# Performance work log

Hardware: AMD Instinct MI355X
Metric: run time of the kernel (lower is better)

The kernel has to match this reference:

```python
import jax, jax.numpy as jnp
import numpy as np

WS = 7        # window_size
SHIFT = 3     # shift_size
HEADS = 6
DIM = 192
HIDDEN = DIM * 6  # mlp_ratio=6
EPS = 1e-5


def _rel_pos_index(ws):
    # static relative-position index, (ws*ws, ws*ws) int
    coords = np.stack(np.meshgrid(np.arange(ws), np.arange(ws), indexing='ij')).reshape(2, -1)
    rel = coords[:, :, None] - coords[:, None, :]            # (2, N, N)
    rel = rel.transpose(1, 2, 0)                             # (N, N, 2)
    rel[:, :, 0] += ws - 1
    rel[:, :, 1] += ws - 1
    rel[:, :, 0] *= 2 * ws - 1
    return rel.sum(-1)


def _layernorm(t, g, b):
    m = t.mean(-1, keepdims=True)
    v = jnp.mean((t - m) ** 2, axis=-1, keepdims=True)
    return (t - m) * jax.lax.rsqrt(v + EPS) * g + b


def setup_inputs() -> dict:
    key = jax.random.key(0)
    ks = jax.random.split(key, 8)
    B, H, W = 16, 56, 56
    x = jax.random.normal(ks[0], (B, H * W, DIM), dtype=jnp.float32)
    p = lambda k, s: (jax.random.normal(k, s, dtype=jnp.float32) * 0.02)
    return {
        'x': x, 'H': H, 'W': W,
        'ln1_g': jnp.ones((DIM,), jnp.float32), 'ln1_b': jnp.zeros((DIM,), jnp.float32),
        'qkv_w': p(ks[1], (3 * DIM, DIM)), 'qkv_b': jnp.zeros((3 * DIM,), jnp.float32),
        'rpb': p(ks[2], ((2 * WS - 1) ** 2, HEADS)),
        'proj_w': p(ks[3], (DIM, DIM)), 'proj_b': jnp.zeros((DIM,), jnp.float32),
        'ln2_g': jnp.ones((DIM,), jnp.float32), 'ln2_b': jnp.zeros((DIM,), jnp.float32),
        'fc1_w': p(ks[4], (HIDDEN, DIM)), 'fc1_b': jnp.zeros((HIDDEN,), jnp.float32),
        'fc2_w': p(ks[5], (DIM, HIDDEN)), 'fc2_b': jnp.zeros((DIM,), jnp.float32),
    }


def reference(x, H, W, ln1_g, ln1_b, qkv_w, qkv_b, rpb, proj_w, proj_b,
              ln2_g, ln2_b, fc1_w, fc1_b, fc2_w, fc2_b):
    B, L, C = x.shape
    hd = C // HEADS
    shortcut = x
    h = _layernorm(x, ln1_g, ln1_b).reshape(B, H, W, C)
    pad_r = (WS - W % WS) % WS
    pad_b = (WS - H % WS) % WS
    h = jnp.pad(h, ((0, 0), (0, pad_b), (0, pad_r), (0, 0)))
    Hp, Wp = H + pad_b, W + pad_r
    if SHIFT > 0:
        h = jnp.roll(h, (-SHIFT, -SHIFT), axis=(1, 2))
    # window partition -> (nW*B, WS*WS, C)
    h = h.reshape(B, Hp // WS, WS, Wp // WS, WS, C).transpose(0, 1, 3, 2, 4, 5)
    h = h.reshape(-1, WS * WS, C)
    nB, N, _ = h.shape
    qkv = (h @ qkv_w.T + qkv_b).reshape(nB, N, 3, HEADS, hd).transpose(2, 0, 3, 1, 4)
    q, k, v = qkv[0], qkv[1], qkv[2]       # (nB, heads, N, hd)
    scale = hd ** -0.5
    attn = jnp.einsum('bhnd,bhmd->bhnm', q * scale, k)
    idx = _rel_pos_index(WS)
    bias = rpb[idx.reshape(-1)].reshape(N, N, HEADS).transpose(2, 0, 1)  # (heads, N, N)
    attn = jax.nn.softmax(attn + bias[None], axis=-1)
    out = jnp.einsum('bhnm,bhmd->bhnd', attn, v).transpose(0, 2, 1, 3).reshape(nB, N, C)
    out = out @ proj_w.T + proj_b
    # window reverse -> (B, Hp, Wp, C)
    out = out.reshape(B, Hp // WS, Wp // WS, WS, WS, C).transpose(0, 1, 3, 2, 4, 5)
    out = out.reshape(B, Hp, Wp, C)
    if SHIFT > 0:
        out = jnp.roll(out, (SHIFT, SHIFT), axis=(1, 2))
    out = out[:, :H, :W, :].reshape(B, H * W, C)
    x = shortcut + out
    h2 = _layernorm(x, ln2_g, ln2_b)
    h2 = jax.nn.gelu(h2 @ fc1_w.T + fc1_b, approximate=False)
    return x + (h2 @ fc2_w.T + fc2_b)
```

## Files before the change

### kernel.cpp

```cpp
#include <hip/hip_runtime.h>

typedef unsigned short u16;
typedef __bf16 bf16x8 __attribute__((ext_vector_type(8)));
typedef __bf16 bf16x2_t __attribute__((ext_vector_type(2)));
typedef float f32x4 __attribute__((ext_vector_type(4)));

#define AS1 __attribute__((address_space(1)))
#define AS3 __attribute__((address_space(3)))

__device__ __forceinline__ void gld16(const void* g, void* l) {
  __builtin_amdgcn_global_load_lds((const AS1 void*)g, (AS3 void*)l, 16, 0, 0);
}

__device__ __forceinline__ u16 f2bf(float f) {
  union { float f; unsigned int u; } v; v.f = f;
  unsigned int u = v.u;
  u += 0x7fffu + ((u >> 16) & 1u);
  return (u16)(u >> 16);
}
__device__ __forceinline__ float bf2f(u16 h) {
  union { unsigned int u; float f; } v; v.u = ((unsigned int)h) << 16; return v.f;
}
__device__ __forceinline__ unsigned int pk2(float a, float b) {
#if __has_builtin(__builtin_amdgcn_cvt_pk_bf16_f32)
  union { bf16x2_t v; unsigned int u; } c;
  c.v = __builtin_amdgcn_cvt_pk_bf16_f32(a, b);
  return c.u;
#else
  return (unsigned int)f2bf(a) | ((unsigned int)f2bf(b) << 16);
#endif
}
__device__ __forceinline__ float gelu_f(float v) {
  float u = v * (1.5957691216f + 0.0713548163f * v * v);
  return v * __builtin_amdgcn_rcpf(1.0f + __expf(-u));
}

__global__ __launch_bounds__(256) void cast_weights(
    const float* __restrict__ w0, const float* __restrict__ w1,
    const float* __restrict__ w2, const float* __restrict__ w3,
    u16* __restrict__ o0, u16* __restrict__ o1,
    u16* __restrict__ o2, u16* __restrict__ o3) {
  int i = blockIdx.x * 256 + threadIdx.x;
  if (i < 110592) o0[i] = f2bf(w0[i]);
  if (i < 36864) {
    int n = i / 192, kp = i - n * 192;
    int h = kp >> 5, dp = kp & 31;
    int d = (dp & 1) ? ((dp >> 1) + 16) : (dp >> 1);
    o1[i] = f2bf(w1[n * 192 + h * 32 + d]);
  }
  if (i < 221184) o2[i] = f2bf(w2[i]);
  if (i < 221184) o3[i] = f2bf(w3[i]);
}

__global__ __launch_bounds__(256) void build_btab(
    const float* __restrict__ rpb, float* __restrict__ btab) {
  int id = blockIdx.x * 256 + threadIdx.x;
  int head = id >> 12;
  int m = (id >> 6) & 63;
  int r = id & 63;
  float v;
  if (m >= 49) v = -1e30f;
  else if (r >= 49) v = 0.0f;
  else {
    int mi = m / 7, mj = m - mi * 7;
    int ri = r / 7, rj = r - ri * 7;
    v = rpb[((ri - mi + 6) * 13 + (rj - mj + 6)) * 6 + head];
  }
  btab[id] = v;
}

__global__ __launch_bounds__(256) void ln_kernel(
    const float* __restrict__ x, const float* __restrict__ g,
    const float* __restrict__ b, u16* __restrict__ out) {
  int row = blockIdx.x * 4 + (threadIdx.x >> 6);
  int lane = threadIdx.x & 63;
  const float* xr = x + (long)row * 192;
  float e0 = xr[lane], e1 = xr[lane + 64], e2 = xr[lane + 128];
  float s = e0 + e1 + e2;
  #pragma unroll
  for (int o = 1; o < 64; o <<= 1) s += __shfl_xor(s, o);
  float mean = s * (1.0f / 192.0f);
  float d0 = e0 - mean, d1 = e1 - mean, d2 = e2 - mean;
  float q = d0 * d0 + d1 * d1 + d2 * d2;
  #pragma unroll
  for (int o = 1; o < 64; o <<= 1) q += __shfl_xor(q, o);
  float rstd = rsqrtf(q * (1.0f / 192.0f) + 1e-5f);
  u16* orow = out + (long)row * 192;
  orow[lane]       = f2bf(d0 * rstd * g[lane]       + b[lane]);
  orow[lane + 64]  = f2bf(d1 * rstd * g[lane + 64]  + b[lane + 64]);
  orow[lane + 128] = f2bf(d2 * rstd * g[lane + 128] + b[lane + 128]);
}

template<int MODE>
__global__ __launch_bounds__(256, 4) void gemm_kernel(
    const u16* __restrict__ A, const u16* __restrict__ W,
    const float* __restrict__ bias, const float* __restrict__ resid,
    void* __restrict__ out, int N, int K) {
  __shared__ u16 lds[2 * 7168];
  float* ct = (float*)lds;
  const int tid = threadIdx.x;
  const int wave = tid >> 6, lane = tid & 63;
  const int wm = wave >> 1, wn = wave & 1;
  const int quad = lane >> 4, l15 = lane & 15;
  const long bm = (long)blockIdx.x * 128;
  const int bn = blockIdx.y * 96;
  const int NC = K >> 5;

  for (int t = wave; t < 14; t += 4) {
    const u16* g = (t < 8)
        ? (A + (bm + t * 16 + l15) * K + quad * 8)
        : (W + (long)(bn + (t - 8) * 16 + l15) * K + quad * 8);
    gld16(g, &lds[t * 512]);
  }
  __syncthreads();

  f32x4 acc[4][3] = {};
  for (int c = 0; c < NC; c++) {
    const int cur = c & 1;
    if (c + 1 < NC) {
      const int kof = (c + 1) * 32 + quad * 8;
      const int nb = (cur ^ 1) * 7168;
      for (int t = wave; t < 14; t += 4) {
        const u16* g = (t < 8)
            ? (A + (bm + t * 16 + l15) * K + kof)
            : (W + (long)(bn + (t - 8) * 16 + l15) * K + kof);
        gld16(g, &lds[nb + t * 512]);
      }
    }
    const u16* buf = lds + cur * 7168;
    bf16x8 af[4], bfr[3];
    #pragma unroll
    for (int mt = 0; mt < 4; mt++)
      af[mt] = *(const bf16x8*)&buf[(wm * 4 + mt) * 512 + lane * 8];
    #pragma unroll
    for (int nt = 0; nt < 3; nt++)
      bfr[nt] = *(const bf16x8*)&buf[(8 + wn * 3 + nt) * 512 + lane * 8];
    #pragma unroll
    for (int mt = 0; mt < 4; mt++)
      #pragma unroll
      for (int nt = 0; nt < 3; nt++)
        acc[mt][nt] = __builtin_amdgcn_mfma_f32_16x16x32_bf16(af[mt], bfr[nt], acc[mt][nt], 0, 0, 0);
    __syncthreads();
  }

  #pragma unroll
  for (int h = 0; h < 2; h++) {
    if (wm == h) {
      #pragma unroll
      for (int nt = 0; nt < 3; nt++) {
        int col = wn * 48 + nt * 16 + l15;
        float bi = bias[bn + col];
        #pragma unroll
        for (int mt = 0; mt < 4; mt++) {
          int row0 = mt * 16 + quad * 4;
          #pragma unroll
          for (int j = 0; j < 4; j++)
            ct[(row0 + j) * 100 + col] = acc[mt][nt][j] + bi;
        }
      }
    }
    __syncthreads();
    #pragma unroll
    for (int it = 0; it < 6; it++) {
      int cc = it * 256 + tid;
      int row = cc / 24, i = cc - row * 24;
      float4 v = *(const float4*)&ct[row * 100 + i * 4];
      long idx = (bm + h * 64 + row) * (long)N + bn + i * 4;
      if (MODE == 2) {
        const float4 rv = *(const float4*)(resid + idx);
        v.x += rv.x; v.y += rv.y; v.z += rv.z; v.w += rv.w;
        *(float4*)((float*)out + idx) = v;
      } else {
        if (MODE == 1) {
          v.x = gelu_f(v.x); v.y = gelu_f(v.y); v.z = gelu_f(v.z); v.w = gelu_f(v.w);
        }
        uint2 pk;
        pk.x = pk2(v.x, v.y);
        pk.y = pk2(v.z, v.w);
        *(uint2*)((u16*)out + idx) = pk;
      }
    }
    if (h == 0) __syncthreads();
  }
}

__global__ __launch_bounds__(256) void attn_kernel(
    const u16* __restrict__ qkv, const float* __restrict__ btab,
    u16* __restrict__ attn) {
  __shared__ u16 lds[4 * 7040];
  int tid = threadIdx.x;
  int wave = tid >> 6, lane = tid & 63;
  int quad = lane >> 4, l15 = lane & 15;
  int w = blockIdx.x * 4 + wave;
  int win = w / 6, head = w - win * 6;
  int b = win >> 6, wy = (win >> 3) & 7, wx = win & 7;
  u16* lp = lds + wave * 7040;
  u16* lvt = lp + 4608;
  float* rsum = (float*)(lp + 6912);

  bf16x8 qb[4], ka[4];
  #pragma unroll
  for (int t = 0; t < 4; t++) {
    int n = t * 16 + l15;
    uint4 qv = {0, 0, 0, 0}, kv = {0, 0, 0, 0}, vv = {0, 0, 0, 0};
    if (n < 49) {
      int i = n / 7, j = n - i * 7;
      int y = wy * 7 + i + 3;  if (y >= 56) y -= 56;
      int xx = wx * 7 + j + 3; if (xx >= 56) xx -= 56;
      long base = ((long)(b * 3136 + y * 56 + xx)) * 576 + head * 32 + quad * 8;
      qv = *(const uint4*)(qkv + base);
      kv = *(const uint4*)(qkv + base + 192);
      vv = *(const uint4*)(qkv + base + 384);
    }
    qb[t] = *(const bf16x8*)&qv;
    ka[t] = *(const bf16x8*)&kv;
    const u16* vp = (const u16*)&vv;
    #pragma unroll
    for (int d = 0; d < 8; d++) lvt[(quad * 8 + d) * 72 + n] = vp[d];
  }

  f32x4 s[4][4];
  const f32x4 fz = {0.0f, 0.0f, 0.0f, 0.0f};
  #pragma unroll
  for (int tm = 0; tm < 4; tm++)
    #pragma unroll
    for (int tr = 0; tr < 4; tr++)
      s[tm][tr] = __builtin_amdgcn_mfma_f32_16x16x32_bf16(ka[tm], qb[tr], fz, 0, 0, 0);

  const float scale = 0.17677669529663687f;
  const float* bt = btab + head * 4096;
  float mx[4] = {-1e30f, -1e30f, -1e30f, -1e30f};
  #pragma unroll
  for (int tm = 0; tm < 4; tm++) {
    int m0 = tm * 16 + quad * 4;
    #pragma unroll
    for (int tr = 0; tr < 4; tr++) {
      int r = tr * 16 + l15;
      #pragma unroll
      for (int j = 0; j < 4; j++) {
        float v = s[tm][tr][j] * scale + bt[(m0 + j) * 64 + r];
        s[tm][tr][j] = v;
        mx[tr] = fmaxf(mx[tr], v);
      }
    }
  }
  #pragma unroll
  for (int tr = 0; tr < 4; tr++) {
    mx[tr] = fmaxf(mx[tr], __shfl_xor(mx[tr], 16));
    mx[tr] = fmaxf(mx[tr], __shfl_xor(mx[tr], 32));
  }
  float sm[4] = {0.f, 0.f, 0.f, 0.f};
  #pragma unroll
  for (int tm = 0; tm < 4; tm++) {
    #pragma unroll
    for (int tr = 0; tr < 4; tr++) {
      int r = tr * 16 + l15;
      float e0 = __expf(s[tm][tr][0] - mx[tr]);
      float e1 = __expf(s[tm][tr][1] - mx[tr]);
      float e2 = __expf(s[tm][tr][2] - mx[tr]);
      float e3 = __expf(s[tm][tr][3] - mx[tr]);
      sm[tr] += (e0 + e1) + (e2 + e3);
      uint2 pk;
      pk.x = pk2(e0, e1);
      pk.y = pk2(e2, e3);
      *(uint2*)&lp[r * 72 + tm * 16 + quad * 4] = pk;
    }
  }
  #pragma unroll
  for (int tr = 0; tr < 4; tr++) {
    sm[tr] += __shfl_xor(sm[tr], 16);
    sm[tr] += __shfl_xor(sm[tr], 32);
  }
  if (quad == 0) {
    #pragma unroll
    for (int tr = 0; tr < 4; tr++) rsum[tr * 16 + l15] = __builtin_amdgcn_rcpf(sm[tr]);
  }

  f32x4 o[4][2] = {};
  #pragma unroll
  for (int ks = 0; ks < 2; ks++) {
    bf16x8 vb0 = *(const bf16x8*)&lvt[(l15) * 72 + ks * 32 + quad * 8];
    bf16x8 vb1 = *(const bf16x8*)&lvt[(16 + l15) * 72 + ks * 32 + quad * 8];
    #pragma unroll
    for (int rt = 0; rt < 4; rt++) {
      bf16x8 pf = *(const bf16x8*)&lp[(rt * 16 + l15) * 72 + ks * 32 + quad * 8];
      o[rt][0] = __builtin_amdgcn_mfma_f32_16x16x32_bf16(pf, vb0, o[rt][0], 0, 0, 0);
      o[rt][1] = __builtin_amdgcn_mfma_f32_16x16x32_bf16(pf, vb1, o[rt][1], 0, 0, 0);
    }
  }
  #pragma unroll
  for (int rt = 0; rt < 4; rt++) {
    #pragma unroll
    for (int j = 0; j < 4; j++) {
      int r = rt * 16 + quad * 4 + j;
      if (r < 49) {
        float inv = rsum[r];
        int i = r / 7, jj = r - i * 7;
        int y = wy * 7 + i + 3;   if (y >= 56) y -= 56;
        int xx = wx * 7 + jj + 3; if (xx >= 56) xx -= 56;
        long base = ((long)(b * 3136 + y * 56 + xx)) * 192 + head * 32 + 2 * l15;
        *(unsigned int*)&attn[base] = pk2(o[rt][0][j] * inv, o[rt][1][j] * inv);
      }
    }
  }
}

extern "C" void kernel_launch(void* const* d_in, const int* in_sizes, int n_in,
                              void* d_out, int out_size, void* d_ws, size_t ws_size,
                              hipStream_t stream) {
  (void)in_sizes; (void)n_in; (void)out_size; (void)ws_size;
  const float* x      = (const float*)d_in[0];
  const float* ln1_g  = (const float*)d_in[3];
  const float* ln1_b  = (const float*)d_in[4];
  const float* qkv_w  = (const float*)d_in[5];
  const float* qkv_b  = (const float*)d_in[6];
  const float* rpb    = (const float*)d_in[7];
  const float* proj_w = (const float*)d_in[8];
  const float* proj_b = (const float*)d_in[9];
  const float* ln2_g  = (const float*)d_in[10];
  const float* ln2_b  = (const float*)d_in[11];
  const float* fc1_w  = (const float*)d_in[12];
  const float* fc1_b  = (const float*)d_in[13];
  const float* fc2_w  = (const float*)d_in[14];
  const float* fc2_b  = (const float*)d_in[15];

  char* ws = (char*)d_ws;
  float* x2   = (float*)(ws + 0);
  u16* hA     = (u16*)(ws + 38535168);
  float* btab = (float*)(ws + 38535168);
  u16* qkv    = (u16*)(ws + 57802752);
  u16* attn   = (u16*)(ws + 115605504);
  u16* hid    = (u16*)(ws + 57802752);
  u16* wbuf   = (u16*)(ws + 173408256);
  u16* qkv_wb  = wbuf;
  u16* proj_wb = wbuf + 110592;
  u16* fc1_wb  = wbuf + 147456;
  u16* fc2_wb  = wbuf + 368640;

  cast_weights<<<dim3(864), 256, 0, stream>>>(qkv_w, proj_w, fc1_w, fc2_w,
                                              qkv_wb, proj_wb, fc1_wb, fc2_wb);
  ln_kernel<<<dim3(12544), 256, 0, stream>>>(x, ln1_g, ln1_b, hA);
  gemm_kernel<0><<<dim3(392, 6), 256, 0, stream>>>(hA, qkv_wb, qkv_b, nullptr,
                                                   qkv, 576, 192);
  build_btab<<<dim3(96), 256, 0, stream>>>(rpb, btab);
  attn_kernel<<<dim3(1536), 256, 0, stream>>>(qkv, btab, attn);
  gemm_kernel<2><<<dim3(392, 2), 256, 0, stream>>>(attn, proj_wb, proj_b, x,
                                                   x2, 192, 192);
  ln_kernel<<<dim3(12544), 256, 0, stream>>>(x2, ln2_g, ln2_b, hA);
  gemm_kernel<1><<<dim3(392, 12), 256, 0, stream>>>(hA, fc1_wb, fc1_b, nullptr,
                                                    hid, 1152, 192);
  gemm_kernel<2><<<dim3(392, 2), 256, 0, stream>>>(hid, fc2_wb, fc2_b, x2,
                                                   (float*)d_out, 192, 1152);
}
```

Before: 344.1 us.

## Triple-buffer GEMM LDS staging with explicit vmcnt waits and a single barrier

Moves the GEMM K-loop from double to triple buffering of the LDS tiles, prefetching two chunks ahead through async global-to-LDS loads. Each wave waits on its own outstanding-load count (vmcnt) instead of a full sync. One barrier per iteration then protects both the read of the current buffer and the reuse of the oldest one. This is meant to hide more global-load latency and cut synchronisation per K step. In exchange LDS use grows and the launch bound drops to 3 blocks per CU, which may lower occupancy.

Measured after the change: 346.7 us. Within noise of the previous version (+0.8%).

```diff
diff --git a/kernel.cpp b/kernel.cpp
--- a/kernel.cpp
+++ b/kernel.cpp
@@ -92,11 +92,11 @@
 }
 
 template<int MODE>
-__global__ __launch_bounds__(256, 4) void gemm_kernel(
+__global__ __launch_bounds__(256, 3) void gemm_kernel(
     const u16* __restrict__ A, const u16* __restrict__ W,
     const float* __restrict__ bias, const float* __restrict__ resid,
     void* __restrict__ out, int N, int K) {
-  __shared__ u16 lds[2 * 7168];
+  __shared__ u16 lds[3 * 7168];
   float* ct = (float*)lds;
   const int tid = threadIdx.x;
   const int wave = tid >> 6, lane = tid & 63;
@@ -106,28 +106,34 @@
   const int bn = blockIdx.y * 96;
   const int NC = K >> 5;
 
-  for (int t = wave; t < 14; t += 4) {
-    const u16* g = (t < 8)
-        ? (A + (bm + t * 16 + l15) * K + quad * 8)
-        : (W + (long)(bn + (t - 8) * 16 + l15) * K + quad * 8);
-    gld16(g, &lds[t * 512]);
-  }
-  __syncthreads();
+  auto stage = [&](int c, int bi) {
+    const int kof = c * 32 + quad * 8;
+    u16* dst = &lds[bi * 7168];
+    for (int t = wave; t < 14; t += 4) {
+      const u16* g = (t < 8)
+          ? (A + (bm + t * 16 + l15) * K + kof)
+          : (W + (long)(bn + (t - 8) * 16 + l15) * K + kof);
+      gld16(g, dst + t * 512);
+    }
+  };
+
+  stage(0, 0);
+  stage(1, 1);
 
   f32x4 acc[4][3] = {};
+  int rb = 0;
+  int sb = 2;
   for (int c = 0; c < NC; c++) {
-    const int cur = c & 1;
     if (c + 1 < NC) {
-      const int kof = (c + 1) * 32 + quad * 8;
-      const int nb = (cur ^ 1) * 7168;
-      for (int t = wave; t < 14; t += 4) {
-        const u16* g = (t < 8)
-            ? (A + (bm + t * 16 + l15) * K + kof)
-            : (W + (long)(bn + (t - 8) * 16 + l15) * K + kof);
-        gld16(g, &lds[nb + t * 512]);
-      }
-    }
-    const u16* buf = lds + cur * 7168;
+      if (wave < 2) asm volatile("s_waitcnt vmcnt(4)" ::: "memory");
+      else          asm volatile("s_waitcnt vmcnt(3)" ::: "memory");
+    } else {
+      asm volatile("s_waitcnt vmcnt(0)" ::: "memory");
+    }
+    __builtin_amdgcn_s_barrier();
+    __builtin_amdgcn_sched_barrier(0);
+    if (c + 2 < NC) stage(c + 2, sb);
+    const u16* buf = lds + rb * 7168;
     bf16x8 af[4], bfr[3];
     #pragma unroll
     for (int mt = 0; mt < 4; mt++)
@@ -140,8 +146,10 @@
       #pragma unroll
       for (int nt = 0; nt < 3; nt++)
         acc[mt][nt] = __builtin_amdgcn_mfma_f32_16x16x32_bf16(af[mt], bfr[nt], acc[mt][nt], 0, 0, 0);
-    __syncthreads();
-  }
+    rb = (rb == 2) ? 0 : rb + 1;
+    sb = (sb == 2) ? 0 : sb + 1;
+  }
+  __syncthreads();
 
   #pragma unroll
   for (int h = 0; h < 2; h++) {
```

## Restructure GEMM: stage full-K weight slabs in LDS, stream A directly to registers

Applied to the files above, without the earlier changes.

The GEMM kernel now loads the whole 192-wide K slab of the weight tile into LDS at once (double-buffered only when K spans several slabs) and reads A fragments straight from global memory into registers with a three-deep rotating prefetch. This removes the per-32-K-chunk LDS staging of A and the barrier in every K step, leaving one barrier per 192-K slab. K becomes a compile-time template parameter. The cost is more LDS and more registers per block, and occupancy is lowered to 3 blocks per CU in launch bounds.

After: 402.8 us. 1.17x slower.

```diff
diff --git a/kernel.cpp b/kernel.cpp
--- a/kernel.cpp
+++ b/kernel.cpp
@@ -91,12 +91,14 @@
   orow[lane + 128] = f2bf(d2 * rstd * g[lane + 128] + b[lane + 128]);
 }
 
-template<int MODE>
-__global__ __launch_bounds__(256, 4) void gemm_kernel(
+template<int MODE, int NM>
+__global__ __launch_bounds__(256, 3) void gemm_kernel(
     const u16* __restrict__ A, const u16* __restrict__ W,
     const float* __restrict__ bias, const float* __restrict__ resid,
-    void* __restrict__ out, int N, int K) {
-  __shared__ u16 lds[2 * 7168];
+    void* __restrict__ out, int N) {
+  constexpr int K = NM * 192;
+  constexpr int NBUF = (NM > 1) ? 2 : 1;
+  __shared__ u16 lds[NBUF * 18432];
   float* ct = (float*)lds;
   const int tid = threadIdx.x;
   const int wave = tid >> 6, lane = tid & 63;
@@ -104,44 +106,63 @@
   const int quad = lane >> 4, l15 = lane & 15;
   const long bm = (long)blockIdx.x * 128;
   const int bn = blockIdx.y * 96;
-  const int NC = K >> 5;
-
-  for (int t = wave; t < 14; t += 4) {
-    const u16* g = (t < 8)
-        ? (A + (bm + t * 16 + l15) * K + quad * 8)
-        : (W + (long)(bn + (t - 8) * 16 + l15) * K + quad * 8);
-    gld16(g, &lds[t * 512]);
-  }
-  __syncthreads();
-
+
+  auto stage = [&](int m, int bi) {
+    u16* dst = &lds[bi * 18432];
+    #pragma unroll
+    for (int i = 0; i < 9; i++) {
+      int t = wave + i * 4;
+      int kc = t / 6, nt = t - kc * 6;
+      const u16* g = W + (long)(bn + nt * 16 + l15) * K + m * 192 + kc * 32 + quad * 8;
+      gld16(g, dst + t * 512);
+    }
+  };
+
+  stage(0, 0);
+
+  const u16* pa0 = A + (bm + wm * 64 + l15) * (long)K + quad * 8;
+  const u16* pa1 = pa0 + 16 * (long)K;
+  const u16* pa2 = pa0 + 32 * (long)K;
+  const u16* pa3 = pa0 + 48 * (long)K;
+
+  bf16x8 ar[3][4];
   f32x4 acc[4][3] = {};
-  for (int c = 0; c < NC; c++) {
-    const int cur = c & 1;
-    if (c + 1 < NC) {
-      const int kof = (c + 1) * 32 + quad * 8;
-      const int nb = (cur ^ 1) * 7168;
-      for (int t = wave; t < 14; t += 4) {
-        const u16* g = (t < 8)
-            ? (A + (bm + t * 16 + l15) * K + kof)
-            : (W + (long)(bn + (t - 8) * 16 + l15) * K + kof);
-        gld16(g, &lds[nb + t * 512]);
-      }
-    }
-    const u16* buf = lds + cur * 7168;
-    bf16x8 af[4], bfr[3];
-    #pragma unroll
-    for (int mt = 0; mt < 4; mt++)
-      af[mt] = *(const bf16x8*)&buf[(wm * 4 + mt) * 512 + lane * 8];
-    #pragma unroll
-    for (int nt = 0; nt < 3; nt++)
-      bfr[nt] = *(const bf16x8*)&buf[(8 + wn * 3 + nt) * 512 + lane * 8];
-    #pragma unroll
-    for (int mt = 0; mt < 4; mt++)
+
+  auto ldA = [&](int s, int off) {
+    ar[s][0] = *(const bf16x8*)(pa0 + off);
+    ar[s][1] = *(const bf16x8*)(pa1 + off);
+    ar[s][2] = *(const bf16x8*)(pa2 + off);
+    ar[s][3] = *(const bf16x8*)(pa3 + off);
+  };
+
+  auto compute = [&](const u16* bb, int last) {
+    #pragma unroll
+    for (int kc = 0; kc < 6; kc++) {
+      bf16x8 bfr[3];
       #pragma unroll
       for (int nt = 0; nt < 3; nt++)
-        acc[mt][nt] = __builtin_amdgcn_mfma_f32_16x16x32_bf16(af[mt], bfr[nt], acc[mt][nt], 0, 0, 0);
+        bfr[nt] = *(const bf16x8*)&bb[(kc * 6 + wn * 3 + nt) * 512 + lane * 8];
+      const int s = kc % 3;
+      #pragma unroll
+      for (int mt = 0; mt < 4; mt++)
+        #pragma unroll
+        for (int nt = 0; nt < 3; nt++)
+          acc[mt][nt] = __builtin_amdgcn_mfma_f32_16x16x32_bf16(ar[s][mt], bfr[nt], acc[mt][nt], 0, 0, 0);
+      if (!last || kc < 3) ldA(s, (kc + 3) * 32);
+    }
+  };
+
+  ldA(0, 0); ldA(1, 32); ldA(2, 64);
+  __syncthreads();
+
+  for (int m = 0; m < NM - 1; m++) {
+    stage(m + 1, (m + 1) & 1);
+    compute(lds + (m & 1) * 18432, 0);
+    pa0 += 192; pa1 += 192; pa2 += 192; pa3 += 192;
     __syncthreads();
   }
+  compute(lds + ((NM - 1) & 1) * 18432, 1);
+  __syncthreads();
 
   #pragma unroll
   for (int h = 0; h < 2; h++) {
@@ -340,15 +361,15 @@
   cast_weights<<<dim3(864), 256, 0, stream>>>(qkv_w, proj_w, fc1_w, fc2_w,
                                               qkv_wb, proj_wb, fc1_wb, fc2_wb);
   ln_kernel<<<dim3(12544), 256, 0, stream>>>(x, ln1_g, ln1_b, hA);
-  gemm_kernel<0><<<dim3(392, 6), 256, 0, stream>>>(hA, qkv_wb, qkv_b, nullptr,
-                                                   qkv, 576, 192);
+  gemm_kernel<0, 1><<<dim3(392, 6), 256, 0, stream>>>(hA, qkv_wb, qkv_b, nullptr,
+                                                      qkv, 576);
   build_btab<<<dim3(96), 256, 0, stream>>>(rpb, btab);
   attn_kernel<<<dim3(1536), 256, 0, stream>>>(qkv, btab, attn);
-  gemm_kernel<2><<<dim3(392, 2), 256, 0, stream>>>(attn, proj_wb, proj_b, x,
-                                                   x2, 192, 192);
+  gemm_kernel<2, 1><<<dim3(392, 2), 256, 0, stream>>>(attn, proj_wb, proj_b, x,
+                                                      x2, 192);
   ln_kernel<<<dim3(12544), 256, 0, stream>>>(x2, ln2_g, ln2_b, hA);
-  gemm_kernel<1><<<dim3(392, 12), 256, 0, stream>>>(hA, fc1_wb, fc1_b, nullptr,
-                                                    hid, 1152, 192);
-  gemm_kernel<2><<<dim3(392, 2), 256, 0, stream>>>(hid, fc2_wb, fc2_b, x2,
-                                                   (float*)d_out, 192, 1152);
-}
+  gemm_kernel<1, 1><<<dim3(392, 12), 256, 0, stream>>>(hA, fc1_wb, fc1_b, nullptr,
+                                                       hid, 1152);
+  gemm_kernel<2, 6><<<dim3(392, 2), 256, 0, stream>>>(hid, fc2_wb, fc2_b, x2,
+                                                      (float*)d_out, 192);
+}
```

## Widen GEMM N-tile to 192 and stage attention bias table in LDS

Applied to the files above, without the earlier changes.

The GEMM kernel now computes a 128x192 output tile per block instead of 128x96. Each wave holds a 4x6 accumulator array, so each A fragment loaded from LDS is reused across twice as many B tiles, and the grids shrink by half in y. The epilogue writes results in four quarter passes through the LDS staging buffer. The attention kernel reorders blocks so all four waves in a block share one head, and it loads that head's bias table once into padded LDS instead of reading it from global memory per element. The trade-offs are higher register pressure and LDS use (launch bounds drop to 3), fewer blocks for the narrow-N GEMMs, and an extra block-wide sync in attention.

New measurement: 340.7 us. About the same (-1.0%).

```diff
diff --git a/kernel.cpp b/kernel.cpp
--- a/kernel.cpp
+++ b/kernel.cpp
@@ -92,95 +92,99 @@
 }
 
 template<int MODE>
-__global__ __launch_bounds__(256, 4) void gemm_kernel(
+__global__ __launch_bounds__(256, 3) void gemm_kernel(
     const u16* __restrict__ A, const u16* __restrict__ W,
     const float* __restrict__ bias, const float* __restrict__ resid,
     void* __restrict__ out, int N, int K) {
-  __shared__ u16 lds[2 * 7168];
+  constexpr int TT = 20;
+  constexpr int BUF = TT * 512;
+  __shared__ u16 lds[2 * BUF];
   float* ct = (float*)lds;
   const int tid = threadIdx.x;
   const int wave = tid >> 6, lane = tid & 63;
   const int wm = wave >> 1, wn = wave & 1;
   const int quad = lane >> 4, l15 = lane & 15;
   const long bm = (long)blockIdx.x * 128;
-  const int bn = blockIdx.y * 96;
+  const int bn = blockIdx.y * 192;
   const int NC = K >> 5;
 
-  for (int t = wave; t < 14; t += 4) {
+  for (int t = wave; t < TT; t += 4) {
     const u16* g = (t < 8)
-        ? (A + (bm + t * 16 + l15) * K + quad * 8)
+        ? (A + (bm + t * 16 + l15) * (long)K + quad * 8)
         : (W + (long)(bn + (t - 8) * 16 + l15) * K + quad * 8);
     gld16(g, &lds[t * 512]);
   }
   __syncthreads();
 
-  f32x4 acc[4][3] = {};
+  f32x4 acc[4][6] = {};
   for (int c = 0; c < NC; c++) {
     const int cur = c & 1;
     if (c + 1 < NC) {
       const int kof = (c + 1) * 32 + quad * 8;
-      const int nb = (cur ^ 1) * 7168;
-      for (int t = wave; t < 14; t += 4) {
+      u16* nb = &lds[(cur ^ 1) * BUF];
+      for (int t = wave; t < TT; t += 4) {
         const u16* g = (t < 8)
-            ? (A + (bm + t * 16 + l15) * K + kof)
+            ? (A + (bm + t * 16 + l15) * (long)K + kof)
             : (W + (long)(bn + (t - 8) * 16 + l15) * K + kof);
-        gld16(g, &lds[nb + t * 512]);
-      }
-    }
-    const u16* buf = lds + cur * 7168;
-    bf16x8 af[4], bfr[3];
+        gld16(g, nb + t * 512);
+      }
+    }
+    const u16* buf = lds + cur * BUF;
+    bf16x8 af[4];
     #pragma unroll
     for (int mt = 0; mt < 4; mt++)
       af[mt] = *(const bf16x8*)&buf[(wm * 4 + mt) * 512 + lane * 8];
     #pragma unroll
-    for (int nt = 0; nt < 3; nt++)
-      bfr[nt] = *(const bf16x8*)&buf[(8 + wn * 3 + nt) * 512 + lane * 8];
-    #pragma unroll
-    for (int mt = 0; mt < 4; mt++)
+    for (int nt = 0; nt < 6; nt++) {
+      bf16x8 bfr = *(const bf16x8*)&buf[(8 + wn * 6 + nt) * 512 + lane * 8];
       #pragma unroll
-      for (int nt = 0; nt < 3; nt++)
-        acc[mt][nt] = __builtin_amdgcn_mfma_f32_16x16x32_bf16(af[mt], bfr[nt], acc[mt][nt], 0, 0, 0);
+      for (int mt = 0; mt < 4; mt++)
+        acc[mt][nt] = __builtin_amdgcn_mfma_f32_16x16x32_bf16(af[mt], bfr, acc[mt][nt], 0, 0, 0);
+    }
     __syncthreads();
   }
 
   #pragma unroll
   for (int h = 0; h < 2; h++) {
-    if (wm == h) {
+    #pragma unroll
+    for (int g = 0; g < 2; g++) {
+      if (wm == h && wn == g) {
+        #pragma unroll
+        for (int nt = 0; nt < 6; nt++) {
+          int col = nt * 16 + l15;
+          float bi = bias[bn + g * 96 + col];
+          #pragma unroll
+          for (int mt = 0; mt < 4; mt++) {
+            int row0 = mt * 16 + quad * 4;
+            #pragma unroll
+            for (int j = 0; j < 4; j++)
+              ct[(row0 + j) * 100 + col] = acc[mt][nt][j] + bi;
+          }
+        }
+      }
+      __syncthreads();
       #pragma unroll
-      for (int nt = 0; nt < 3; nt++) {
-        int col = wn * 48 + nt * 16 + l15;
-        float bi = bias[bn + col];
-        #pragma unroll
-        for (int mt = 0; mt < 4; mt++) {
-          int row0 = mt * 16 + quad * 4;
-          #pragma unroll
-          for (int j = 0; j < 4; j++)
-            ct[(row0 + j) * 100 + col] = acc[mt][nt][j] + bi;
+      for (int it = 0; it < 6; it++) {
+        int cc = it * 256 + tid;
+        int row = cc / 24, i = cc - row * 24;
+        float4 v = *(const float4*)&ct[row * 100 + i * 4];
+        long idx = (bm + h * 64 + row) * (long)N + bn + g * 96 + i * 4;
+        if (MODE == 2) {
+          const float4 rv = *(const float4*)(resid + idx);
+          v.x += rv.x; v.y += rv.y; v.z += rv.z; v.w += rv.w;
+          *(float4*)((float*)out + idx) = v;
+        } else {
+          if (MODE == 1) {
+            v.x = gelu_f(v.x); v.y = gelu_f(v.y); v.z = gelu_f(v.z); v.w = gelu_f(v.w);
+          }
+          uint2 pk;
+          pk.x = pk2(v.x, v.y);
+          pk.y = pk2(v.z, v.w);
+          *(uint2*)((u16*)out + idx) = pk;
         }
       }
-    }
-    __syncthreads();
-    #pragma unroll
-    for (int it = 0; it < 6; it++) {
-      int cc = it * 256 + tid;
-      int row = cc / 24, i = cc - row * 24;
-      float4 v = *(const float4*)&ct[row * 100 + i * 4];
-      long idx = (bm + h * 64 + row) * (long)N + bn + i * 4;
-      if (MODE == 2) {
-        const float4 rv = *(const float4*)(resid + idx);
-        v.x += rv.x; v.y += rv.y; v.z += rv.z; v.w += rv.w;
-        *(float4*)((float*)out + idx) = v;
-      } else {
-        if (MODE == 1) {
-          v.x = gelu_f(v.x); v.y = gelu_f(v.y); v.z = gelu_f(v.z); v.w = gelu_f(v.w);
-        }
-        uint2 pk;
-        pk.x = pk2(v.x, v.y);
-        pk.y = pk2(v.z, v.w);
-        *(uint2*)((u16*)out + idx) = pk;
-      }
-    }
-    if (h == 0) __syncthreads();
+      if (!(h == 1 && g == 1)) __syncthreads();
+    }
   }
 }
 
@@ -188,15 +192,28 @@
     const u16* __restrict__ qkv, const float* __restrict__ btab,
     u16* __restrict__ attn) {
   __shared__ u16 lds[4 * 7040];
+  __shared__ float sbias[64 * 65];
   int tid = threadIdx.x;
   int wave = tid >> 6, lane = tid & 63;
   int quad = lane >> 4, l15 = lane & 15;
-  int w = blockIdx.x * 4 + wave;
-  int win = w / 6, head = w - win * 6;
+  int head = blockIdx.x % 6;
+  int grp = blockIdx.x / 6;
+  int win = grp * 4 + wave;
   int b = win >> 6, wy = (win >> 3) & 7, wx = win & 7;
   u16* lp = lds + wave * 7040;
   u16* lvt = lp + 4608;
   float* rsum = (float*)(lp + 6912);
+
+  {
+    const float* bsrc = btab + head * 4096;
+    #pragma unroll
+    for (int i = 0; i < 4; i++) {
+      int idx4 = tid + i * 256;
+      float4 v = *(const float4*)(bsrc + idx4 * 4);
+      float* dst = &sbias[(idx4 >> 4) * 65 + (idx4 & 15) * 4];
+      dst[0] = v.x; dst[1] = v.y; dst[2] = v.z; dst[3] = v.w;
+    }
+  }
 
   bf16x8 qb[4], ka[4];
   #pragma unroll
@@ -227,8 +244,9 @@
     for (int tr = 0; tr < 4; tr++)
       s[tm][tr] = __builtin_amdgcn_mfma_f32_16x16x32_bf16(ka[tm], qb[tr], fz, 0, 0, 0);
 
+  __syncthreads();
+
   const float scale = 0.17677669529663687f;
-  const float* bt = btab + head * 4096;
   float mx[4] = {-1e30f, -1e30f, -1e30f, -1e30f};
   #pragma unroll
   for (int tm = 0; tm < 4; tm++) {
@@ -238,7 +256,7 @@
       int r = tr * 16 + l15;
       #pragma unroll
       for (int j = 0; j < 4; j++) {
-        float v = s[tm][tr][j] * scale + bt[(m0 + j) * 64 + r];
+        float v = s[tm][tr][j] * scale + sbias[(m0 + j) * 65 + r];
         s[tm][tr][j] = v;
         mx[tr] = fmaxf(mx[tr], v);
       }
@@ -340,15 +358,15 @@
   cast_weights<<<dim3(864), 256, 0, stream>>>(qkv_w, proj_w, fc1_w, fc2_w,
                                               qkv_wb, proj_wb, fc1_wb, fc2_wb);
   ln_kernel<<<dim3(12544), 256, 0, stream>>>(x, ln1_g, ln1_b, hA);
-  gemm_kernel<0><<<dim3(392, 6), 256, 0, stream>>>(hA, qkv_wb, qkv_b, nullptr,
+  gemm_kernel<0><<<dim3(392, 3), 256, 0, stream>>>(hA, qkv_wb, qkv_b, nullptr,
                                                    qkv, 576, 192);
   build_btab<<<dim3(96), 256, 0, stream>>>(rpb, btab);
   attn_kernel<<<dim3(1536), 256, 0, stream>>>(qkv, btab, attn);
-  gemm_kernel<2><<<dim3(392, 2), 256, 0, stream>>>(attn, proj_wb, proj_b, x,
+  gemm_kernel<2><<<dim3(392, 1), 256, 0, stream>>>(attn, proj_wb, proj_b, x,
                                                    x2, 192, 192);
   ln_kernel<<<dim3(12544), 256, 0, stream>>>(x2, ln2_g, ln2_b, hA);
-  gemm_kernel<1><<<dim3(392, 12), 256, 0, stream>>>(hA, fc1_wb, fc1_b, nullptr,
-                                                    hid, 1152, 192);
-  gemm_kernel<2><<<dim3(392, 2), 256, 0, stream>>>(hid, fc2_wb, fc2_b, x2,
+  gemm_kernel<1><<<dim3(392, 6), 256, 0, stream>>>(hA, fc1_wb, fc1_b, nullptr,
+                                                   hid, 1152, 192);
+  gemm_kernel<2><<<dim3(392, 1), 256, 0, stream>>>(hid, fc2_wb, fc2_b, x2,
                                                    (float*)d_out, 192, 1152);
 }
```
